# Kernel tuning notes

Measured on AMD Instinct MI355X. Metric: run time of the kernel, lower is better.

Reference implementation:

```python
import jax, jax.numpy as jnp
import numpy as np

EPS = 1e-5


def _binary_act(x):
    # Forward: sign(x). Backward: piecewise-polynomial surrogate (ApproxSign STE).
    out3 = jnp.where(x < -1, -1.0,
            jnp.where(x < 0, x * x + 2.0 * x,
             jnp.where(x < 1, -x * x + 2.0 * x, 1.0)))
    return jax.lax.stop_gradient(jnp.sign(x) - out3) + out3


def _binarize_weights(w):
    # Per-output-channel scaling factor (detached), forward = scale*sign(w),
    # backward flows through clamp(w, -1, 1) (STE).
    scale = jax.lax.stop_gradient(jnp.mean(jnp.abs(w), axis=(1, 2, 3), keepdims=True))
    clipped = jnp.clip(w, -1.0, 1.0)
    return jax.lax.stop_gradient(scale * jnp.sign(w) - clipped) + clipped


def setup_inputs() -> dict:
    key = jax.random.key(0)
    kx, kw = jax.random.split(key)
    B, Cin, Cout, H, W = 32, 128, 128, 56, 56
    x = jax.random.normal(kx, (B, Cin, H, W), dtype=jnp.float32)
    # HardBinaryConv: weight = rand(n)*0.001 permuted then reshaped -> just random in [0, 0.001)
    w = jax.random.uniform(kw, (Cout, Cin, 3, 3), dtype=jnp.float32) * 0.001
    return {
        "x": x,
        "bias0": jnp.zeros((Cin,), jnp.float32),   # move0 LearnableBias
        "w": w,                                     # HardBinaryConv latent weights
        "gamma": jnp.ones((Cout,), jnp.float32),    # BN weight
        "beta": jnp.zeros((Cout,), jnp.float32),    # BN bias
        "bias1": jnp.zeros((Cout,), jnp.float32),   # move1
        "alpha": jnp.full((Cout,), 0.25, jnp.float32),  # PReLU per-channel
        "bias2": jnp.zeros((Cout,), jnp.float32),   # move2
    }


def reference(x, bias0, w, gamma, beta, bias1, alpha, bias2):
    def pc(v):  # per-channel broadcast (1, C, 1, 1)
        return v[None, :, None, None]

    residual = x
    out = x + pc(bias0)                     # move0
    out = _binary_act(out)                  # binary activation
    bw = _binarize_weights(w)               # {-scale, +scale} weights
    y = jax.lax.conv_general_dilated(
        out, bw, window_strides=(1, 1), padding=((1, 1), (1, 1)),
        dimension_numbers=("NCHW", "OIHW", "NCHW"))
    # BatchNorm2d (training mode: biased batch statistics over N,H,W)
    mean = jnp.mean(y, axis=(0, 2, 3), keepdims=True)
    var = jnp.mean(jnp.square(y - mean), axis=(0, 2, 3), keepdims=True)
    y = (y - mean) * jax.lax.rsqrt(var + EPS) * pc(gamma) + pc(beta)
    y = y + residual
    y = y + pc(bias1)                       # move1
    y = jnp.where(y >= 0, y, pc(alpha) * y)  # PReLU
    y = y + pc(bias2)                       # move2
    return y
```

## Files before the change

kernel.cpp:

```cpp
#include <hip/hip_runtime.h>
#include <stdint.h>

#define NB 32
#define NC 128
#define NH 56
#define NW 56
#define NHW_ (NH * NW)
#define NPIX (NB * NHW_)
#define NO 128
#define NK 1152
#define NSTRIP 14

typedef unsigned long long u64;

__global__ __launch_bounds__(256) void pack_act(const float* __restrict__ x,
                                                const float* __restrict__ bias0,
                                                u64* __restrict__ packA) {
    int p = blockIdx.x * 256 + threadIdx.x;
    if (p >= NPIX) return;
    int n = p / NHW_;
    int rem = p - n * NHW_;
    const float* xb = x + (size_t)n * NC * NHW_ + rem;
    u64 w0 = 0, w1 = 0;
#pragma unroll 8
    for (int c = 0; c < 64; ++c)
        w0 |= (u64)((xb[(size_t)c * NHW_] + bias0[c]) > 0.f) << c;
#pragma unroll 8
    for (int c = 0; c < 64; ++c)
        w1 |= (u64)((xb[(size_t)(c + 64) * NHW_] + bias0[c + 64]) > 0.f) << c;
    packA[(size_t)p * 2]     = w0;
    packA[(size_t)p * 2 + 1] = w1;
}

__global__ __launch_bounds__(64) void pack_wgt(const float* __restrict__ w,
                                               u64* __restrict__ packW,
                                               float* __restrict__ scaleW,
                                               int* __restrict__ corrW) {
    __shared__ u64 sb[18];
    int o = blockIdx.x;
    int t = threadIdx.x;
    const float* wo = w + (size_t)o * NK;
    float s = 0.f;
    for (int i = t; i < NK; i += 64) s += fabsf(wo[i]);
    for (int off = 32; off; off >>= 1) s += __shfl_down(s, off);
    if (t == 0) scaleW[o] = s / (float)NK;
    if (t < 18) {
        int tap = t >> 1;
        int j   = t & 1;
        u64 bits = 0;
        for (int cc = 0; cc < 64; ++cc) {
            int c = j * 64 + cc;
            bits |= (u64)(wo[c * 9 + tap] > 0.f) << cc;
        }
        packW[(size_t)o * 18 + t] = bits;
        sb[t] = bits;
    }
    __syncthreads();
    if (t == 0) {
        int cv[9];
#pragma unroll
        for (int tap = 0; tap < 9; ++tap)
            cv[tap] = NC - 2 * (__popcll(sb[2 * tap]) + __popcll(sb[2 * tap + 1]));
        int* cw = corrW + o * 8;
        cw[0] = cv[0] + cv[3] + cv[6];
        cw[1] = cv[2] + cv[5] + cv[8];
        cw[2] = cv[0] + cv[1] + cv[2];
        cw[3] = cv[6] + cv[7] + cv[8];
        cw[4] = cv[0];
        cw[5] = cv[2];
        cw[6] = cv[6];
        cw[7] = cv[8];
    }
}

__global__ __launch_bounds__(256, 4) void conv_bin(const u64* __restrict__ packA,
                                                   const u64* __restrict__ packW,
                                                   const int* __restrict__ corrW,
                                                   short* __restrict__ yI) {
    __shared__ u64 lw[64 * 18];
    __shared__ int lc[64 * 8];

    int bid = blockIdx.x;
    int n = bid / (NSTRIP * 2);
    int rem = bid - n * (NSTRIP * 2);
    int strip = rem >> 1;
    int chh = rem & 1;
    int obase = chh * 64;
    int h0 = strip * 4;

    for (int i = threadIdx.x; i < 64 * 18; i += 256) lw[i] = packW[(size_t)obase * 18 + i];
    for (int i = threadIdx.x; i < 64 * 8; i += 256) lc[i] = corrW[obase * 8 + i];

    int wv = threadIdx.x >> 6, lane = threadIdx.x & 63;
    bool act = lane < NW;
    bool top = (strip == 0), bot = (strip == NSTRIP - 1);

    u64 a[6][3][2];
    bool cvv[3];
    cvv[0] = act && (lane >= 1);
    cvv[1] = act;
    cvv[2] = act && (lane + 1 < NW);
#pragma unroll
    for (int r = 0; r < 6; ++r) {
        int hi = h0 - 1 + r;
        bool rvv = (hi >= 0) && (hi < NH);
        int hc = hi < 0 ? 0 : (hi >= NH ? NH - 1 : hi);
#pragma unroll
        for (int c = 0; c < 3; ++c) {
            int wi = lane - 1 + c;
            int wc = wi < 0 ? 0 : (wi >= NW ? NW - 1 : wi);
            ulonglong2 q = *reinterpret_cast<const ulonglong2*>(
                packA + ((size_t)n * NHW_ + (size_t)hc * NW + wc) * 2);
            bool v = rvv && cvv[c];
            a[r][c][0] = v ? q.x : 0;
            a[r][c][1] = v ? q.y : 0;
        }
    }
    __syncthreads();

    bool isL = (lane == 0), isR = (lane == NW - 1);
    short* ybase = yI + (size_t)n * NO * NHW_ + (size_t)h0 * NW + lane;

    for (int oo = 0; oo < 16; ++oo) {
        int lo = (wv << 4) + oo;
        int o = obase + lo;
        const u64* wp = &lw[lo * 18];
        int pc0 = 0, pc1 = 0, pc2 = 0, pc3 = 0;
#pragma unroll
        for (int kh = 0; kh < 3; ++kh) {
#pragma unroll
            for (int kw = 0; kw < 3; ++kw) {
                u64 w0 = wp[(kh * 3 + kw) * 2];
                u64 w1 = wp[(kh * 3 + kw) * 2 + 1];
                pc0 += __popcll(a[0 + kh][kw][0] ^ w0) + __popcll(a[0 + kh][kw][1] ^ w1);
                pc1 += __popcll(a[1 + kh][kw][0] ^ w0) + __popcll(a[1 + kh][kw][1] ^ w1);
                pc2 += __popcll(a[2 + kh][kw][0] ^ w0) + __popcll(a[2 + kh][kw][1] ^ w1);
                pc3 += __popcll(a[3 + kh][kw][0] ^ w0) + __popcll(a[3 + kh][kw][1] ^ w1);
            }
        }
        const int* cw = &lc[lo * 8];
        int corrcol = isL ? cw[0] : (isR ? cw[1] : 0);
        int base = NK - corrcol;
        int d0 = base - 2 * pc0;
        int d1 = base - 2 * pc1;
        int d2 = base - 2 * pc2;
        int d3 = base - 2 * pc3;
        if (top) d0 -= cw[2] - (isL ? cw[4] : (isR ? cw[5] : 0));
        if (bot) d3 -= cw[3] - (isL ? cw[6] : (isR ? cw[7] : 0));
        if (act) {
            short* yp = ybase + (size_t)o * NHW_;
            yp[0]      = (short)d0;
            yp[NW]     = (short)d1;
            yp[2 * NW] = (short)d2;
            yp[3 * NW] = (short)d3;
        }
    }
}

__global__ __launch_bounds__(256) void stats_coef(const short* __restrict__ yI,
                                                  const float* __restrict__ scaleW,
                                                  const float* __restrict__ gamma,
                                                  const float* __restrict__ beta,
                                                  const float* __restrict__ bias1,
                                                  float* __restrict__ coefA,
                                                  float* __restrict__ coefB) {
    int o = blockIdx.x;
    long long s = 0, sq = 0;
    for (int v = threadIdx.x; v < 12544; v += 256) {
        int n = v / 392, off = v - n * 392;
        const int4 pv = *reinterpret_cast<const int4*>(
            yI + ((size_t)n * NO + o) * NHW_ + (size_t)off * 8);
        int qs[4] = {pv.x, pv.y, pv.z, pv.w};
#pragma unroll
        for (int j = 0; j < 4; ++j) {
            int lo = (int)(short)(qs[j] & 0xffff);
            int hi = (int)(qs[j] >> 16);
            s += lo + hi;
            sq += (long long)(lo * lo + hi * hi);
        }
    }
    __shared__ long long ls[256];
    __shared__ long long lq[256];
    int tid = threadIdx.x;
    ls[tid] = s; lq[tid] = sq;
    __syncthreads();
    for (int st = 128; st; st >>= 1) {
        if (tid < st) { ls[tid] += ls[tid + st]; lq[tid] += lq[tid + st]; }
        __syncthreads();
    }
    if (tid == 0) {
        double cnt = (double)NPIX;
        double mean = (double)ls[0] / cnt;
        double var = (double)lq[0] / cnt - mean * mean;
        if (var < 0.0) var = 0.0;
        float sc = scaleW[o];
        float rs = rsqrtf((float)((double)sc * (double)sc * var) + 1e-5f);
        float g = gamma[o];
        coefA[o] = sc * g * rs;
        coefB[o] = beta[o] - (float)((double)sc * mean) * g * rs + bias1[o];
    }
}

__global__ __launch_bounds__(256) void final_store(const short* __restrict__ yI,
                                                   const float* __restrict__ x,
                                                   const float* __restrict__ coefA,
                                                   const float* __restrict__ coefB,
                                                   const float* __restrict__ alpha,
                                                   const float* __restrict__ bias2,
                                                   float* __restrict__ out) {
    const size_t ngroups = (size_t)NB * NO * NHW_ / 8;
    for (size_t g = (size_t)blockIdx.x * blockDim.x + threadIdx.x; g < ngroups;
         g += (size_t)gridDim.x * blockDim.x) {
        size_t i = g * 8;
        int o = (int)((i / NHW_) % NO);
        float a = coefA[o], bb = coefB[o], al = alpha[o], b2 = bias2[o];
        int4 yv = *reinterpret_cast<const int4*>(yI + i);
        float4 x0 = *reinterpret_cast<const float4*>(x + i);
        float4 x1 = *reinterpret_cast<const float4*>(x + i + 4);
        int q[4] = {yv.x, yv.y, yv.z, yv.w};
        float xs[8] = {x0.x, x0.y, x0.z, x0.w, x1.x, x1.y, x1.z, x1.w};
        float r[8];
#pragma unroll
        for (int j = 0; j < 4; ++j) {
            float lo = (float)(short)(q[j] & 0xffff);
            float hi = (float)(q[j] >> 16);
            float t0 = fmaf(a, lo, bb) + xs[2 * j];
            float t1 = fmaf(a, hi, bb) + xs[2 * j + 1];
            t0 = t0 >= 0.f ? t0 : al * t0;
            t1 = t1 >= 0.f ? t1 : al * t1;
            r[2 * j]     = t0 + b2;
            r[2 * j + 1] = t1 + b2;
        }
        float4 o0 = {r[0], r[1], r[2], r[3]};
        float4 o1 = {r[4], r[5], r[6], r[7]};
        *reinterpret_cast<float4*>(out + i)     = o0;
        *reinterpret_cast<float4*>(out + i + 4) = o1;
    }
}

__device__ inline void load_nbhd(const u64* __restrict__ packA, int n, int h,
                                 int wcol, bool act, u64 a[9][2], unsigned* vmask) {
    unsigned m = 0;
#pragma unroll
    for (int kh = 0; kh < 3; ++kh) {
        int hi = h + kh - 1;
        bool vh = (hi >= 0) && (hi < NH);
#pragma unroll
        for (int kw = 0; kw < 3; ++kw) {
            int wi = wcol + kw - 1;
            int t = kh * 3 + kw;
            bool v = act && vh && (wi >= 0) && (wi < NW);
            int hc = hi < 0 ? 0 : (hi >= NH ? NH - 1 : hi);
            int wc = wi < 0 ? 0 : (wi >= NW ? NW - 1 : wi);
            size_t idx = ((size_t)n * NHW_ + (size_t)hc * NW + wc) * 2;
            u64 q0 = packA[idx], q1 = packA[idx + 1];
            a[t][0] = v ? q0 : 0;
            a[t][1] = v ? q1 : 0;
            m |= (unsigned)v << t;
        }
    }
    *vmask = m;
}

__global__ __launch_bounds__(256) void conv_stats_atomic(const u64* __restrict__ packA,
                                                         const u64* __restrict__ packW,
                                                         int* __restrict__ sumI,
                                                         u64* __restrict__ sumsqI) {
    __shared__ u64 lw[NO * 18];
    for (int i = threadIdx.x; i < NO * 18; i += 256) lw[i] = packW[i];
    int nh = blockIdx.x;
    int n = nh / NH, h = nh - n * NH;
    int wave = threadIdx.x >> 6, lane = threadIdx.x & 63;
    bool act = lane < NW;
    u64 a[9][2]; unsigned vm;
    load_nbhd(packA, n, h, lane, act, a, &vm);
    __syncthreads();
    for (int oo = 0; oo < 32; ++oo) {
        int o = (wave << 5) + oo;
        int dot = 0;
#pragma unroll
        for (int t = 0; t < 9; ++t) {
            int pc = __popcll(a[t][0] ^ lw[(o * 9 + t) * 2]) +
                     __popcll(a[t][1] ^ lw[(o * 9 + t) * 2 + 1]);
            dot += ((vm >> t) & 1) ? (NC - 2 * pc) : 0;
        }
        int s = dot, sq = dot * dot;
        for (int off = 32; off; off >>= 1) {
            s  += __shfl_down(s, off);
            sq += __shfl_down(sq, off);
        }
        if (lane == 0) {
            atomicAdd(&sumI[o], s);
            atomicAdd(&sumsqI[o], (u64)(unsigned)sq);
        }
    }
}

__global__ __launch_bounds__(128) void bn_coef(const int* __restrict__ sumP,
                                               const u64* __restrict__ sqP,
                                               const float* __restrict__ scaleW,
                                               const float* __restrict__ gamma,
                                               const float* __restrict__ beta,
                                               const float* __restrict__ bias1,
                                               float* __restrict__ coefA,
                                               float* __restrict__ coefB) {
    int o = threadIdx.x;
    double cnt = (double)NPIX;
    double mean = (double)sumP[o] / cnt;
    double var = (double)sqP[o] / cnt - mean * mean;
    if (var < 0.0) var = 0.0;
    float sc = scaleW[o];
    float rs = rsqrtf((float)((double)sc * (double)sc * var) + 1e-5f);
    float g = gamma[o];
    coefA[o] = sc * g * rs;
    coefB[o] = beta[o] - (float)((double)sc * mean) * g * rs + bias1[o];
}

__global__ __launch_bounds__(256) void final_recompute(const u64* __restrict__ packA,
                                                       const u64* __restrict__ packW,
                                                       const float* __restrict__ coefA,
                                                       const float* __restrict__ coefB,
                                                       const float* __restrict__ alpha,
                                                       const float* __restrict__ bias2,
                                                       const float* __restrict__ x,
                                                       float* __restrict__ out) {
    __shared__ u64 lw[NO * 18];
    for (int i = threadIdx.x; i < NO * 18; i += 256) lw[i] = packW[i];
    int nh = blockIdx.x;
    int n = nh / NH, h = nh - n * NH;
    int wave = threadIdx.x >> 6, lane = threadIdx.x & 63;
    bool act = lane < NW;
    u64 a[9][2]; unsigned vm;
    load_nbhd(packA, n, h, lane, act, a, &vm);
    __syncthreads();
    for (int oo = 0; oo < 32; ++oo) {
        int o = (wave << 5) + oo;
        int dot = 0;
#pragma unroll
        for (int t = 0; t < 9; ++t) {
            int pc = __popcll(a[t][0] ^ lw[(o * 9 + t) * 2]) +
                     __popcll(a[t][1] ^ lw[(o * 9 + t) * 2 + 1]);
            dot += ((vm >> t) & 1) ? (NC - 2 * pc) : 0;
        }
        if (act) {
            size_t idx = ((size_t)n * NO + o) * NHW_ + (size_t)h * NW + lane;
            float t = fmaf(coefA[o], (float)dot, coefB[o]) + x[idx];
            t = t >= 0.f ? t : alpha[o] * t;
            out[idx] = t + bias2[o];
        }
    }
}

extern "C" void kernel_launch(void* const* d_in, const int* in_sizes, int n_in,
                              void* d_out, int out_size, void* d_ws, size_t ws_size,
                              hipStream_t stream) {
    (void)in_sizes; (void)n_in; (void)out_size;
    const float* x     = (const float*)d_in[0];
    const float* bias0 = (const float*)d_in[1];
    const float* w     = (const float*)d_in[2];
    const float* gamma = (const float*)d_in[3];
    const float* beta  = (const float*)d_in[4];
    const float* bias1 = (const float*)d_in[5];
    const float* alpha = (const float*)d_in[6];
    const float* bias2 = (const float*)d_in[7];
    float* out = (float*)d_out;
    char* ws = (char*)d_ws;

    u64*   packA  = (u64*)ws;
    u64*   packW  = (u64*)(ws + 1605632);
    int*   corrW  = (int*)(ws + 1624064);
    float* scaleW = (float*)(ws + 1628160);
    float* coefA  = (float*)(ws + 1628672);
    float* coefB  = (float*)(ws + 1629184);
    int*   sumP   = (int*)(ws + 1629696);
    u64*   sqP    = (u64*)(ws + 1630208);
    short* yI     = (short*)(ws + 1631232);
    bool store = ws_size >= (size_t)1631232 + (size_t)NB * NO * NHW_ * 2;

    pack_act<<<NPIX / 256, 256, 0, stream>>>(x, bias0, packA);
    pack_wgt<<<NO, 64, 0, stream>>>(w, packW, scaleW, corrW);

    if (store) {
        conv_bin<<<NB * NSTRIP * 2, 256, 0, stream>>>(packA, packW, corrW, yI);
        stats_coef<<<NO, 256, 0, stream>>>(yI, scaleW, gamma, beta, bias1, coefA, coefB);
        final_store<<<2048, 256, 0, stream>>>(yI, x, coefA, coefB, alpha, bias2, out);
    } else {
        hipMemsetAsync(sumP, 0, 512 + 1024, stream);
        conv_stats_atomic<<<NB * NH, 256, 0, stream>>>(packA, packW, sumP, sqP);
        bn_coef<<<1, NO, 0, stream>>>(sumP, sqP, scaleW, gamma, beta, bias1, coefA, coefB);
        final_recompute<<<NB * NH, 256, 0, stream>>>(packA, packW, coefA, coefB, alpha, bias2, x, out);
    }
}
```

Before: 109.9 us.

## Fuse BN statistics into binary conv via per-strip partial sums

The conv kernel now computes per-channel sum and sum-of-squares of its integer outputs with wavefront shuffles and writes them as deterministic partials, one per (channel, image, strip) slot. A small reduction kernel then replaces the old stats pass that re-read the whole int16 conv output. The conv grid also moves from 2 to 4 channel groups per strip, so each block loads fewer weights and the grid has more blocks, with the occupancy hint lowered from 4 to 3. The cost is that each block redundantly reloads its activation tile across twice as many channel groups, and workspace offsets are shifted.

```diff
diff --git a/kernel.cpp b/kernel.cpp
--- a/kernel.cpp
+++ b/kernel.cpp
@@ -10,6 +10,7 @@
 #define NO 128
 #define NK 1152
 #define NSTRIP 14
+#define NSLOT (NB * NSTRIP)
 
 typedef unsigned long long u64;
 
@@ -73,23 +74,25 @@
     }
 }
 
-__global__ __launch_bounds__(256, 4) void conv_bin(const u64* __restrict__ packA,
+__global__ __launch_bounds__(256, 3) void conv_bin(const u64* __restrict__ packA,
                                                    const u64* __restrict__ packW,
                                                    const int* __restrict__ corrW,
-                                                   short* __restrict__ yI) {
-    __shared__ u64 lw[64 * 18];
-    __shared__ int lc[64 * 8];
+                                                   short* __restrict__ yI,
+                                                   int* __restrict__ sumP,
+                                                   int* __restrict__ sqP) {
+    __shared__ u64 lw[32 * 18];
+    __shared__ int lc[32 * 8];
 
     int bid = blockIdx.x;
-    int n = bid / (NSTRIP * 2);
-    int rem = bid - n * (NSTRIP * 2);
-    int strip = rem >> 1;
-    int chh = rem & 1;
-    int obase = chh * 64;
+    int n = bid / (NSTRIP * 4);
+    int rem = bid - n * (NSTRIP * 4);
+    int strip = rem >> 2;
+    int cg = rem & 3;
+    int obase = cg * 32;
     int h0 = strip * 4;
 
-    for (int i = threadIdx.x; i < 64 * 18; i += 256) lw[i] = packW[(size_t)obase * 18 + i];
-    for (int i = threadIdx.x; i < 64 * 8; i += 256) lc[i] = corrW[obase * 8 + i];
+    for (int i = threadIdx.x; i < 32 * 18; i += 256) lw[i] = packW[(size_t)obase * 18 + i];
+    if (threadIdx.x < 32 * 8) lc[threadIdx.x] = corrW[obase * 8 + threadIdx.x];
 
     int wv = threadIdx.x >> 6, lane = threadIdx.x & 63;
     bool act = lane < NW;
@@ -120,9 +123,10 @@
 
     bool isL = (lane == 0), isR = (lane == NW - 1);
     short* ybase = yI + (size_t)n * NO * NHW_ + (size_t)h0 * NW + lane;
-
-    for (int oo = 0; oo < 16; ++oo) {
-        int lo = (wv << 4) + oo;
+    int sl = n * NSTRIP + strip;
+
+    for (int oo = 0; oo < 8; ++oo) {
+        int lo = (wv << 3) + oo;
         int o = obase + lo;
         const u64* wp = &lw[lo * 18];
         int pc0 = 0, pc1 = 0, pc2 = 0, pc3 = 0;
@@ -154,44 +158,44 @@
             yp[2 * NW] = (short)d2;
             yp[3 * NW] = (short)d3;
         }
-    }
-}
-
-__global__ __launch_bounds__(256) void stats_coef(const short* __restrict__ yI,
-                                                  const float* __restrict__ scaleW,
-                                                  const float* __restrict__ gamma,
-                                                  const float* __restrict__ beta,
-                                                  const float* __restrict__ bias1,
-                                                  float* __restrict__ coefA,
-                                                  float* __restrict__ coefB) {
+        int s = act ? (d0 + d1 + d2 + d3) : 0;
+        int q = act ? (d0 * d0 + d1 * d1 + d2 * d2 + d3 * d3) : 0;
+#pragma unroll
+        for (int off = 32; off; off >>= 1) {
+            s += __shfl_down(s, off);
+            q += __shfl_down(q, off);
+        }
+        if (lane == 0) {
+            sumP[o * NSLOT + sl] = s;
+            sqP[o * NSLOT + sl]  = q;
+        }
+    }
+}
+
+__global__ __launch_bounds__(64) void bn_coef2(const int* __restrict__ sumP,
+                                               const int* __restrict__ sqP,
+                                               const float* __restrict__ scaleW,
+                                               const float* __restrict__ gamma,
+                                               const float* __restrict__ beta,
+                                               const float* __restrict__ bias1,
+                                               float* __restrict__ coefA,
+                                               float* __restrict__ coefB) {
     int o = blockIdx.x;
-    long long s = 0, sq = 0;
-    for (int v = threadIdx.x; v < 12544; v += 256) {
-        int n = v / 392, off = v - n * 392;
-        const int4 pv = *reinterpret_cast<const int4*>(
-            yI + ((size_t)n * NO + o) * NHW_ + (size_t)off * 8);
-        int qs[4] = {pv.x, pv.y, pv.z, pv.w};
-#pragma unroll
-        for (int j = 0; j < 4; ++j) {
-            int lo = (int)(short)(qs[j] & 0xffff);
-            int hi = (int)(qs[j] >> 16);
-            s += lo + hi;
-            sq += (long long)(lo * lo + hi * hi);
-        }
-    }
-    __shared__ long long ls[256];
-    __shared__ long long lq[256];
-    int tid = threadIdx.x;
-    ls[tid] = s; lq[tid] = sq;
-    __syncthreads();
-    for (int st = 128; st; st >>= 1) {
-        if (tid < st) { ls[tid] += ls[tid + st]; lq[tid] += lq[tid + st]; }
-        __syncthreads();
-    }
-    if (tid == 0) {
+    int t = threadIdx.x;
+    long long s = 0, q = 0;
+    for (int i = t; i < NSLOT; i += 64) {
+        s += sumP[o * NSLOT + i];
+        q += sqP[o * NSLOT + i];
+    }
+#pragma unroll
+    for (int off = 32; off; off >>= 1) {
+        s += __shfl_down(s, off);
+        q += __shfl_down(q, off);
+    }
+    if (t == 0) {
         double cnt = (double)NPIX;
-        double mean = (double)ls[0] / cnt;
-        double var = (double)lq[0] / cnt - mean * mean;
+        double mean = (double)s / cnt;
+        double var = (double)q / cnt - mean * mean;
         if (var < 0.0) var = 0.0;
         float sc = scaleW[o];
         float rs = rsqrtf((float)((double)sc * (double)sc * var) + 1e-5f);
@@ -372,22 +376,24 @@
     float* scaleW = (float*)(ws + 1628160);
     float* coefA  = (float*)(ws + 1628672);
     float* coefB  = (float*)(ws + 1629184);
-    int*   sumP   = (int*)(ws + 1629696);
-    u64*   sqP    = (u64*)(ws + 1630208);
-    short* yI     = (short*)(ws + 1631232);
-    bool store = ws_size >= (size_t)1631232 + (size_t)NB * NO * NHW_ * 2;
+    int*   sumI   = (int*)(ws + 1629696);
+    u64*   sqI    = (u64*)(ws + 1630208);
+    int*   sumP   = (int*)(ws + 1631232);
+    int*   sqP    = (int*)(ws + 1860608);
+    short* yI     = (short*)(ws + 2089984);
+    bool store = ws_size >= (size_t)2089984 + (size_t)NB * NO * NHW_ * 2;
 
     pack_act<<<NPIX / 256, 256, 0, stream>>>(x, bias0, packA);
     pack_wgt<<<NO, 64, 0, stream>>>(w, packW, scaleW, corrW);
 
     if (store) {
-        conv_bin<<<NB * NSTRIP * 2, 256, 0, stream>>>(packA, packW, corrW, yI);
-        stats_coef<<<NO, 256, 0, stream>>>(yI, scaleW, gamma, beta, bias1, coefA, coefB);
+        conv_bin<<<NB * NSTRIP * 4, 256, 0, stream>>>(packA, packW, corrW, yI, sumP, sqP);
+        bn_coef2<<<NO, 64, 0, stream>>>(sumP, sqP, scaleW, gamma, beta, bias1, coefA, coefB);
         final_store<<<2048, 256, 0, stream>>>(yI, x, coefA, coefB, alpha, bias2, out);
     } else {
-        hipMemsetAsync(sumP, 0, 512 + 1024, stream);
-        conv_stats_atomic<<<NB * NH, 256, 0, stream>>>(packA, packW, sumP, sqP);
-        bn_coef<<<1, NO, 0, stream>>>(sumP, sqP, scaleW, gamma, beta, bias1, coefA, coefB);
+        hipMemsetAsync(sumI, 0, 512 + 1024, stream);
+        conv_stats_atomic<<<NB * NH, 256, 0, stream>>>(packA, packW, sumI, sqI);
+        bn_coef<<<1, NO, 0, stream>>>(sumI, sqI, scaleW, gamma, beta, bias1, coefA, coefB);
         final_recompute<<<NB * NH, 256, 0, stream>>>(packA, packW, coefA, coefB, alpha, bias2, x, out);
     }
 }
```

New measurement: 93.34 us. 15.1% less time.
